# Kernel tuning notes

Measured on AMD Instinct MI355X. Metric: run time of the kernel, lower is better.

## Reference

```python
import jax, jax.numpy as jnp
import numpy as np

EPS = 1e-7        # keras backend epsilon
ALPHA = 0.25
GAMMA = 2.0
NEG_INF = -1e30

B, T, V, L = 256, 1024, 128, 64
BLANK = V - 1     # blank_index=-1 in tf ctc_loss_v2


def setup_inputs() -> dict:
    key = jax.random.key(0)
    k1, k2 = jax.random.split(key)
    y_pred = jax.random.uniform(k1, (B, T, V), dtype=jnp.float32)
    y_true = jax.random.randint(k2, (B, L), 0, V - 1, dtype=jnp.int32)
    return {"y_true": y_true, "y_pred": y_pred}


def _ctc_neg_log_lik(y_true, y_pred):
    """Standard CTC forward (alpha) DP in log space; full lengths T and L."""
    b, t, v = y_pred.shape
    l = y_true.shape[1]
    s = 2 * l + 1
    # tf ctc_loss_v2 log-softmaxes its logits; logits here are log(y_pred+eps)
    logp = jax.nn.log_softmax(jnp.log(y_pred + EPS), axis=-1)     # [B,T,V]
    # extended label sequence: blank, l1, blank, l2, ..., blank    [B,S]
    ext = jnp.full((b, s), BLANK, dtype=y_true.dtype)
    ext = ext.at[:, 1::2].set(y_true)
    # per-timestep log-probs of extended labels -> [T,B,S]
    lp_ext = jnp.take_along_axis(logp, ext[:, None, :], axis=2)   # [B,T,S]
    lp_ext = jnp.transpose(lp_ext, (1, 0, 2))                     # [T,B,S]
    # skip transition s-2 -> s allowed iff ext[s] != blank and ext[s] != ext[s-2]
    ext_sm2 = jnp.pad(ext[:, :-2], ((0, 0), (2, 0)), constant_values=BLANK)
    allow_skip = (ext != BLANK) & (ext != ext_sm2)                # [B,S]

    alpha0 = jnp.full((b, s), NEG_INF, dtype=logp.dtype)
    alpha0 = alpha0.at[:, 0].set(lp_ext[0, :, 0])
    alpha0 = alpha0.at[:, 1].set(lp_ext[0, :, 1])

    def step(alpha, lp_t):
        a0 = alpha
        a1 = jnp.pad(alpha[:, :-1], ((0, 0), (1, 0)), constant_values=NEG_INF)
        a2 = jnp.pad(alpha[:, :-2], ((0, 0), (2, 0)), constant_values=NEG_INF)
        a2 = jnp.where(allow_skip, a2, NEG_INF)
        m = jnp.maximum(jnp.maximum(a0, a1), a2)                  # stable LSE
        lse = m + jnp.log(jnp.exp(a0 - m) + jnp.exp(a1 - m) + jnp.exp(a2 - m))
        return lse + lp_t, None

    alphaT, _ = jax.lax.scan(step, alpha0, lp_ext[1:])
    log_lik = jnp.logaddexp(alphaT[:, -1], alphaT[:, -2])         # [B]
    return -log_lik


def reference(y_true, y_pred):
    loss = _ctc_neg_log_lik(y_true, y_pred)                       # [B]
    p = jnp.exp(-loss)
    focal = ALPHA * (1.0 - p) ** GAMMA * loss
    return jnp.mean(focal)
```

## Files before the change

kernel.cpp:

```cpp
#include <hip/hip_runtime.h>


#define EPSF 1e-7f

constexpr int Bb = 256;
constexpr int Tt = 1024;
constexpr int Vv = 128;
constexpr int Ll = 64;

template <int Ctrl, int RowMask, int BankMask, bool BoundCtrl>
__device__ __forceinline__ float dppf(float x) {
    return __int_as_float(__builtin_amdgcn_update_dpp(
        0, __float_as_int(x), Ctrl, RowMask, BankMask, BoundCtrl));
}

__device__ __forceinline__ float wave_sum63(float x) {
    x += dppf<0x111, 0xf, 0xf, true>(x);
    x += dppf<0x112, 0xf, 0xf, true>(x);
    x += dppf<0x114, 0xf, 0xf, true>(x);
    x += dppf<0x118, 0xf, 0xf, true>(x);
    x += dppf<0x142, 0xa, 0xf, false>(x);
    x += dppf<0x143, 0xc, 0xf, false>(x);
    return x;
}

__device__ __forceinline__ float half_sum(float x) {
    x += dppf<0x111, 0xf, 0xf, true>(x);
    x += dppf<0x112, 0xf, 0xf, true>(x);
    x += dppf<0x114, 0xf, 0xf, true>(x);
    x += dppf<0x118, 0xf, 0xf, true>(x);
    x += dppf<0x142, 0xa, 0xf, false>(x);
    return x;
}

__device__ __forceinline__ float wave_max63(float x) {
    x = fmaxf(x, dppf<0x111, 0xf, 0xf, true>(x));
    x = fmaxf(x, dppf<0x112, 0xf, 0xf, true>(x));
    x = fmaxf(x, dppf<0x114, 0xf, 0xf, true>(x));
    x = fmaxf(x, dppf<0x118, 0xf, 0xf, true>(x));
    x = fmaxf(x, dppf<0x142, 0xa, 0xf, false>(x));
    x = fmaxf(x, dppf<0x143, 0xc, 0xf, false>(x));
    return x;
}

__device__ __forceinline__ float bcast63(float x) {
    return __int_as_float(__builtin_amdgcn_readlane(__float_as_int(x), 63));
}

#define DO_STEP(QE, QB, CHK)                                                 \
    do {                                                                     \
        const float am1_ = dppf<0x138, 0xf, 0xf, true>(a_odd);               \
        const float ne_  = (a_even + am1_) * (QB);                           \
        const float no_  = fmaf(maskf, am1_, a_odd + a_even) * (QE);         \
        const float n1_  = (a128 + a_odd) * (QB);                            \
        a_even = ne_; a_odd = no_; a128 = n1_;                               \
        if (CHK) {                                                           \
            const float m_ = fmaxf(fmaxf(a_even, a_odd), a128);              \
            if (__all(m_ < 0x1p-75f)) {                                      \
                const float    wmax_  = bcast63(wave_max63(m_));             \
                const unsigned e_     = __float_as_uint(wmax_) >> 23;        \
                const float    scale_ = __uint_as_float((254u - e_) << 23);  \
                eacc += (int)e_ - 127;                                       \
                a_even *= scale_; a_odd *= scale_; a128 *= scale_;           \
            }                                                                \
        }                                                                    \
    } while (0)

#define CSTEP(J, GQ, BQ, CHK)                                                \
    do {                                                                     \
        const float qe_ = GQ + EPSF, qb_ = BQ + EPSF;                        \
        const int   tn_ = t0 + 16 + (J);                                     \
        GQ = ygl[tn_ * Vv + lab];                                            \
        BQ = ygl[tn_ * Vv + (Vv - 1)];                                       \
        DO_STEP(qe_, qb_, CHK);                                              \
    } while (0)

__launch_bounds__(1024, 1)
__global__ void fused_kernel(const int* __restrict__ y_true,
                             const float* __restrict__ y_pred,
                             float* __restrict__ focal_ws) {
    const int b    = blockIdx.x;
    const int lane = threadIdx.x & 63;
    const int wv   = threadIdx.x >> 6;

    const float*  ygl = y_pred + (size_t)b * Tt * Vv;
    const float4* yb4 = (const float4*)ygl;

    __shared__ float part[30];

    if (wv >= 1) {
        const int hw2 = 2 * (wv - 1) + (lane >> 5);
        const int c32 = lane & 31;
        float ll = 0.0f;
#pragma unroll 5
        for (int k = 0; k < 35; ++k) {
            const int r  = hw2 + 30 * k;
            const int rc = (r < Tt) ? r : (Tt - 1);
            const float4 v = yb4[rc * (Vv / 4) + c32];
            const float  s = half_sum(v.x + v.y + v.z + v.w);
            if (r < Tt && c32 == 31)
                ll += __log2f(s + (float)Vv * EPSF);
        }
        if (c32 == 31) part[hw2] = ll;
    } else {
        const int lab = y_true[b * Ll + lane];
        const int labp = __shfl_up(lab, 1);
        const float maskf = (lane == 0 || lab != labp) ? 1.0f : 0.0f;
        float a_even = (lane == 0) ? 1.0f : 0.0f;
        float a_odd = 0.0f, a128 = 0.0f;
        int   eacc = 0;

        __builtin_amdgcn_s_setprio(1);
        float gq0  = ygl[0 * Vv + lab],  bq0  = ygl[0 * Vv + Vv - 1];
        float gq1  = ygl[1 * Vv + lab],  bq1  = ygl[1 * Vv + Vv - 1];
        float gq2  = ygl[2 * Vv + lab],  bq2  = ygl[2 * Vv + Vv - 1];
        float gq3  = ygl[3 * Vv + lab],  bq3  = ygl[3 * Vv + Vv - 1];
        float gq4  = ygl[4 * Vv + lab],  bq4  = ygl[4 * Vv + Vv - 1];
        float gq5  = ygl[5 * Vv + lab],  bq5  = ygl[5 * Vv + Vv - 1];
        float gq6  = ygl[6 * Vv + lab],  bq6  = ygl[6 * Vv + Vv - 1];
        float gq7  = ygl[7 * Vv + lab],  bq7  = ygl[7 * Vv + Vv - 1];
        float gq8  = ygl[8 * Vv + lab],  bq8  = ygl[8 * Vv + Vv - 1];
        float gq9  = ygl[9 * Vv + lab],  bq9  = ygl[9 * Vv + Vv - 1];
        float gq10 = ygl[10 * Vv + lab], bq10 = ygl[10 * Vv + Vv - 1];
        float gq11 = ygl[11 * Vv + lab], bq11 = ygl[11 * Vv + Vv - 1];
        float gq12 = ygl[12 * Vv + lab], bq12 = ygl[12 * Vv + Vv - 1];
        float gq13 = ygl[13 * Vv + lab], bq13 = ygl[13 * Vv + Vv - 1];
        float gq14 = ygl[14 * Vv + lab], bq14 = ygl[14 * Vv + Vv - 1];
        float gq15 = ygl[15 * Vv + lab], bq15 = ygl[15 * Vv + Vv - 1];

        for (int t0 = 0; t0 < Tt - 16; t0 += 16) {
            CSTEP(0,  gq0,  bq0,  false);
            CSTEP(1,  gq1,  bq1,  false);
            CSTEP(2,  gq2,  bq2,  false);
            CSTEP(3,  gq3,  bq3,  false);
            CSTEP(4,  gq4,  bq4,  false);
            CSTEP(5,  gq5,  bq5,  false);
            CSTEP(6,  gq6,  bq6,  false);
            CSTEP(7,  gq7,  bq7,  false);
            CSTEP(8,  gq8,  bq8,  false);
            CSTEP(9,  gq9,  bq9,  false);
            CSTEP(10, gq10, bq10, false);
            CSTEP(11, gq11, bq11, false);
            CSTEP(12, gq12, bq12, false);
            CSTEP(13, gq13, bq13, false);
            CSTEP(14, gq14, bq14, false);
            CSTEP(15, gq15, bq15, true);
        }
        DO_STEP(gq0 + EPSF,  bq0 + EPSF,  false);
        DO_STEP(gq1 + EPSF,  bq1 + EPSF,  false);
        DO_STEP(gq2 + EPSF,  bq2 + EPSF,  false);
        DO_STEP(gq3 + EPSF,  bq3 + EPSF,  false);
        DO_STEP(gq4 + EPSF,  bq4 + EPSF,  false);
        DO_STEP(gq5 + EPSF,  bq5 + EPSF,  false);
        DO_STEP(gq6 + EPSF,  bq6 + EPSF,  false);
        DO_STEP(gq7 + EPSF,  bq7 + EPSF,  false);
        DO_STEP(gq8 + EPSF,  bq8 + EPSF,  false);
        DO_STEP(gq9 + EPSF,  bq9 + EPSF,  false);
        DO_STEP(gq10 + EPSF, bq10 + EPSF, false);
        DO_STEP(gq11 + EPSF, bq11 + EPSF, false);
        DO_STEP(gq12 + EPSF, bq12 + EPSF, false);
        DO_STEP(gq13 + EPSF, bq13 + EPSF, false);
        DO_STEP(gq14 + EPSF, bq14 + EPSF, false);
        DO_STEP(gq15 + EPSF, bq15 + EPSF, true);
        __builtin_amdgcn_s_setprio(0);

        __syncthreads();

        float vs = (lane < 30) ? part[lane] : 0.0f;
        vs = wave_sum63(vs);
        if (lane == 63) {
            const float acc_ld  = vs;
            const float tot     = fmaxf(a128 + a_odd, 1e-37f);
            const float log2lik = __log2f(tot) + (float)eacc - acc_ld;
            const float ln_lik  = 0.69314718055994530942f * log2lik;
            const float loss    = -ln_lik;
            const float pp      = __expf(ln_lik);
            const float om      = 1.0f - pp;
            focal_ws[b] = 0.25f * om * om * loss;
        }
        return;
    }
    __syncthreads();
}

__global__ void finalize_kernel(const float* __restrict__ focal_ws,
                                float* __restrict__ out) {
    const int i    = threadIdx.x;
    const int lane = i & 63;
    const int wv   = i >> 6;

    float f = focal_ws[i];
#pragma unroll
    for (int off = 32; off > 0; off >>= 1) f += __shfl_xor(f, off);

    __shared__ float red[4];
    if (lane == 0) red[wv] = f;
    __syncthreads();
    if (i == 0)
        out[0] = (red[0] + red[1] + red[2] + red[3]) * (1.0f / (float)Bb);
}

extern "C" void kernel_launch(void* const* d_in, const int* in_sizes, int n_in,
                              void* d_out, int out_size, void* d_ws, size_t ws_size,
                              hipStream_t stream) {
    const int*   y_true = (const int*)d_in[0];
    const float* y_pred = (const float*)d_in[1];
    float* focal_ws = (float*)d_ws;

    fused_kernel<<<Bb, 1024, 0, stream>>>(y_true, y_pred, focal_ws);
    finalize_kernel<<<1, 256, 0, stream>>>(focal_ws, (float*)d_out);
}
```

Before: 228.0 us.

## Stage CTC gather through double-buffered LDS with producer waves and per-chunk barriers

Splits the block into three roles. Wave 0 runs the serial CTC recurrence. Waves 1-2 gather label and blank probabilities for each 64-timestep chunk into a double-buffered shared-memory tile. Waves 3-15 compute the row log-sum normaliser chunk by chunk. This takes the global-memory gather latency off the recurrence's critical path, since the recurrence now reads from LDS. The cost is 17 block-wide barriers, with the DP wave waiting on the producers at each phase, plus one extra pipeline phase.

```diff
diff --git a/kernel.cpp b/kernel.cpp
--- a/kernel.cpp
+++ b/kernel.cpp
@@ -3,10 +3,14 @@
 
 #define EPSF 1e-7f
 
-constexpr int Bb = 256;
-constexpr int Tt = 1024;
-constexpr int Vv = 128;
-constexpr int Ll = 64;
+constexpr int Bb  = 256;
+constexpr int Tt  = 1024;
+constexpr int Vv  = 128;
+constexpr int Ll  = 64;
+constexpr int CH  = 64;
+constexpr int NCH = Tt / CH;
+constexpr int NPH = NCH + 1;
+constexpr int NSH = 26;
 
 template <int Ctrl, int RowMask, int BankMask, bool BoundCtrl>
 __device__ __forceinline__ float dppf(float x) {
@@ -66,15 +70,6 @@
         }                                                                    \
     } while (0)
 
-#define CSTEP(J, GQ, BQ, CHK)                                                \
-    do {                                                                     \
-        const float qe_ = GQ + EPSF, qb_ = BQ + EPSF;                        \
-        const int   tn_ = t0 + 16 + (J);                                     \
-        GQ = ygl[tn_ * Vv + lab];                                            \
-        BQ = ygl[tn_ * Vv + (Vv - 1)];                                       \
-        DO_STEP(qe_, qb_, CHK);                                              \
-    } while (0)
-
 __launch_bounds__(1024, 1)
 __global__ void fused_kernel(const int* __restrict__ y_true,
                              const float* __restrict__ y_pred,
@@ -86,87 +81,89 @@
     const float*  ygl = y_pred + (size_t)b * Tt * Vv;
     const float4* yb4 = (const float4*)ygl;
 
-    __shared__ float part[30];
-
-    if (wv >= 1) {
-        const int hw2 = 2 * (wv - 1) + (lane >> 5);
-        const int c32 = lane & 31;
-        float ll = 0.0f;
-#pragma unroll 5
-        for (int k = 0; k < 35; ++k) {
-            const int r  = hw2 + 30 * k;
-            const int rc = (r < Tt) ? r : (Tt - 1);
-            const float4 v = yb4[rc * (Vv / 4) + c32];
-            const float  s = half_sum(v.x + v.y + v.z + v.w);
-            if (r < Tt && c32 == 31)
-                ll += __log2f(s + (float)Vv * EPSF);
+    __shared__ float4 gt4[2 * (CH / 4) * 64];
+    __shared__ float4 bk4[2 * (CH / 4)];
+    __shared__ float  part[NSH];
+
+    int lab = 0;
+    if (wv <= 2) lab = y_true[b * Ll + lane];
+
+    float a_even = 0.0f, a_odd = 0.0f, a128 = 0.0f, maskf = 0.0f;
+    int   eacc = 0;
+    if (wv == 0) {
+        const int labp = __shfl_up(lab, 1);
+        maskf  = (lane == 0 || lab != labp) ? 1.0f : 0.0f;
+        a_even = (lane == 0) ? 1.0f : 0.0f;
+    }
+
+    const int h   = 2 * (wv - 3) + (lane >> 5);
+    const int c32 = lane & 31;
+    float ll = 0.0f;
+
+    for (int p = 0; p < NPH; ++p) {
+        if (wv >= 3) {
+            if (p < NCH) {
+                const float4* src4 = yb4 + p * CH * (Vv / 4);
+                const float4 v0 = src4[h * 32 + c32];
+                const float4 v1 = src4[(h + 26) * 32 + c32];
+                const float  s0 = half_sum(v0.x + v0.y + v0.z + v0.w);
+                const float  s1 = half_sum(v1.x + v1.y + v1.z + v1.w);
+                if (c32 == 31)
+                    ll += __log2f(s0 + (float)Vv * EPSF) +
+                          __log2f(s1 + (float)Vv * EPSF);
+                if (h < 12) {
+                    const float4 v2 = src4[(h + 52) * 32 + c32];
+                    const float  s2 = half_sum(v2.x + v2.y + v2.z + v2.w);
+                    if (c32 == 31) ll += __log2f(s2 + (float)Vv * EPSF);
+                }
+            } else if (c32 == 31) {
+                part[h] = ll;
+            }
+        } else if (wv >= 1) {
+            if (p < NCH) {
+                const int    tg0 = (wv - 1) * 32;
+                const float* src = ygl + p * CH * Vv;
+                float* gtw = (float*)(gt4 + (p & 1) * (CH / 4) * 64);
+#pragma unroll 8
+                for (int j = 0; j < 32; ++j) {
+                    const int tl = tg0 + j;
+                    gtw[(tl >> 2) * 256 + lane * 4 + (tl & 3)] =
+                        src[tl * Vv + lab];
+                }
+                if (lane < 32) {
+                    const int tl = tg0 + lane;
+                    ((float*)(bk4 + (p & 1) * (CH / 4)))[tl] =
+                        src[tl * Vv + (Vv - 1)];
+                }
+            }
+        } else {
+            const int c = p - 1;
+            if (c >= 0) {
+                __builtin_amdgcn_s_setprio(1);
+                const float4* gbf = gt4 + (c & 1) * (CH / 4) * 64;
+                const float4* bbf = bk4 + (c & 1) * (CH / 4);
+                float4 gA = gbf[0 * 64 + lane], gB = gbf[1 * 64 + lane];
+                float4 bA = bbf[0],             bB = bbf[1];
+#pragma unroll
+                for (int i = 0; i < 16; ++i) {
+                    DO_STEP(gA.x + EPSF, bA.x + EPSF, false);
+                    DO_STEP(gA.y + EPSF, bA.y + EPSF, false);
+                    DO_STEP(gA.z + EPSF, bA.z + EPSF, false);
+                    DO_STEP(gA.w + EPSF, bA.w + EPSF, (i & 3) == 3);
+                    gA = gB; bA = bB;
+                    if (i < 14) {
+                        gB = gbf[(i + 2) * 64 + lane];
+                        bB = bbf[i + 2];
+                    }
+                }
+                __builtin_amdgcn_s_setprio(0);
+            }
         }
-        if (c32 == 31) part[hw2] = ll;
-    } else {
-        const int lab = y_true[b * Ll + lane];
-        const int labp = __shfl_up(lab, 1);
-        const float maskf = (lane == 0 || lab != labp) ? 1.0f : 0.0f;
-        float a_even = (lane == 0) ? 1.0f : 0.0f;
-        float a_odd = 0.0f, a128 = 0.0f;
-        int   eacc = 0;
-
-        __builtin_amdgcn_s_setprio(1);
-        float gq0  = ygl[0 * Vv + lab],  bq0  = ygl[0 * Vv + Vv - 1];
-        float gq1  = ygl[1 * Vv + lab],  bq1  = ygl[1 * Vv + Vv - 1];
-        float gq2  = ygl[2 * Vv + lab],  bq2  = ygl[2 * Vv + Vv - 1];
-        float gq3  = ygl[3 * Vv + lab],  bq3  = ygl[3 * Vv + Vv - 1];
-        float gq4  = ygl[4 * Vv + lab],  bq4  = ygl[4 * Vv + Vv - 1];
-        float gq5  = ygl[5 * Vv + lab],  bq5  = ygl[5 * Vv + Vv - 1];
-        float gq6  = ygl[6 * Vv + lab],  bq6  = ygl[6 * Vv + Vv - 1];
-        float gq7  = ygl[7 * Vv + lab],  bq7  = ygl[7 * Vv + Vv - 1];
-        float gq8  = ygl[8 * Vv + lab],  bq8  = ygl[8 * Vv + Vv - 1];
-        float gq9  = ygl[9 * Vv + lab],  bq9  = ygl[9 * Vv + Vv - 1];
-        float gq10 = ygl[10 * Vv + lab], bq10 = ygl[10 * Vv + Vv - 1];
-        float gq11 = ygl[11 * Vv + lab], bq11 = ygl[11 * Vv + Vv - 1];
-        float gq12 = ygl[12 * Vv + lab], bq12 = ygl[12 * Vv + Vv - 1];
-        float gq13 = ygl[13 * Vv + lab], bq13 = ygl[13 * Vv + Vv - 1];
-        float gq14 = ygl[14 * Vv + lab], bq14 = ygl[14 * Vv + Vv - 1];
-        float gq15 = ygl[15 * Vv + lab], bq15 = ygl[15 * Vv + Vv - 1];
-
-        for (int t0 = 0; t0 < Tt - 16; t0 += 16) {
-            CSTEP(0,  gq0,  bq0,  false);
-            CSTEP(1,  gq1,  bq1,  false);
-            CSTEP(2,  gq2,  bq2,  false);
-            CSTEP(3,  gq3,  bq3,  false);
-            CSTEP(4,  gq4,  bq4,  false);
-            CSTEP(5,  gq5,  bq5,  false);
-            CSTEP(6,  gq6,  bq6,  false);
-            CSTEP(7,  gq7,  bq7,  false);
-            CSTEP(8,  gq8,  bq8,  false);
-            CSTEP(9,  gq9,  bq9,  false);
-            CSTEP(10, gq10, bq10, false);
-            CSTEP(11, gq11, bq11, false);
-            CSTEP(12, gq12, bq12, false);
-            CSTEP(13, gq13, bq13, false);
-            CSTEP(14, gq14, bq14, false);
-            CSTEP(15, gq15, bq15, true);
-        }
-        DO_STEP(gq0 + EPSF,  bq0 + EPSF,  false);
-        DO_STEP(gq1 + EPSF,  bq1 + EPSF,  false);
-        DO_STEP(gq2 + EPSF,  bq2 + EPSF,  false);
-        DO_STEP(gq3 + EPSF,  bq3 + EPSF,  false);
-        DO_STEP(gq4 + EPSF,  bq4 + EPSF,  false);
-        DO_STEP(gq5 + EPSF,  bq5 + EPSF,  false);
-        DO_STEP(gq6 + EPSF,  bq6 + EPSF,  false);
-        DO_STEP(gq7 + EPSF,  bq7 + EPSF,  false);
-        DO_STEP(gq8 + EPSF,  bq8 + EPSF,  false);
-        DO_STEP(gq9 + EPSF,  bq9 + EPSF,  false);
-        DO_STEP(gq10 + EPSF, bq10 + EPSF, false);
-        DO_STEP(gq11 + EPSF, bq11 + EPSF, false);
-        DO_STEP(gq12 + EPSF, bq12 + EPSF, false);
-        DO_STEP(gq13 + EPSF, bq13 + EPSF, false);
-        DO_STEP(gq14 + EPSF, bq14 + EPSF, false);
-        DO_STEP(gq15 + EPSF, bq15 + EPSF, true);
-        __builtin_amdgcn_s_setprio(0);
-
         __syncthreads();
-
-        float vs = (lane < 30) ? part[lane] : 0.0f;
+    }
+
+    if (wv == 0) {
+        float vs = (lane < NSH) ? part[lane] : 0.0f;
         vs = wave_sum63(vs);
         if (lane == 63) {
             const float acc_ld  = vs;
@@ -178,9 +175,7 @@
             const float om      = 1.0f - pp;
             focal_ws[b] = 0.25f * om * om * loss;
         }
-        return;
     }
-    __syncthreads();
 }
 
 __global__ void finalize_kernel(const float* __restrict__ focal_ws,
```

Result: faster. 198.5 us (-12.9%).
